# Kernel optimization log

Hardware: AMD Instinct MI355X
Metric: run time of the kernel (lower is better)

The kernel has to match this reference:

```python
import jax, jax.numpy as jnp
import numpy as np

NUM_HEADS = 8


def setup_inputs() -> dict:
    key = jax.random.key(0)
    k1, k2, k3 = jax.random.split(key, 3)
    B, N, C = 4, 2048, 256
    x = jax.random.normal(k1, (B, N, C), dtype=jnp.float32)
    qkv_w = jax.random.normal(k2, (3 * C, C), dtype=jnp.float32) * (C ** -0.5)
    proj_w = jax.random.normal(k3, (C, C), dtype=jnp.float32) * (C ** -0.5)
    proj_b = jnp.zeros((C,), dtype=jnp.float32)
    return {"x": x, "qkv_w": qkv_w, "proj_w": proj_w, "proj_b": proj_b}


def reference(x, qkv_w, proj_w, proj_b):
    B, N, C = x.shape
    H = NUM_HEADS
    hd = C // H
    scale = hd ** -0.5
    # 1x1 conv over [B,C,N,1] == per-token linear: [B,3C,N]
    qkv = jnp.einsum('bnc,dc->bdn', x, qkv_w)
    # faithful to torch reshape+chunk: per-head interleaved q/k/v layout
    qkv = qkv.reshape(B, H, 3 * hd, N)
    q, k, v = jnp.split(qkv, 3, axis=2)  # each [B,H,hd,N]
    # attn[b,h,i,j] = sum_d k[b,h,d,i] * q[b,h,d,j], scaled
    attn = jnp.einsum('bhdi,bhdj->bhij', k, q) * scale  # [B,H,Nk,Nq]
    attn = jax.nn.softmax(attn, axis=-2)  # softmax over key axis (dim=-2)
    out = jnp.einsum('bhdi,bhij->bhdj', v, attn)  # [B,H,hd,N]
    out = out.reshape(B, C, N, 1)
    # proj 1x1 conv with bias
    out = jnp.einsum('bcnq,dc->bdnq', out, proj_w) + proj_b[None, :, None, None]
    return out
```

## Files before the change

kernel.cpp:

```cpp
#include <hip/hip_runtime.h>
#include <hip/hip_bf16.h>

#define NTOK 2048
#define CDIM 256
#define HEADS 8
#define HD 32
#define QSC 0.25505480068568306f

typedef __attribute__((ext_vector_type(8))) short short8;
typedef __attribute__((ext_vector_type(4))) float float4v;
typedef unsigned short ushort_t;
typedef unsigned int uint_t;

#define MFMA(a, b, c) __builtin_amdgcn_mfma_f32_16x16x32_bf16(a, b, c, 0, 0, 0)

__device__ __forceinline__ uint_t cvt_pk(float lo, float hi) {
    uint_t r;
    asm("v_cvt_pk_bf16_f32 %0, %1, %2" : "=v"(r) : "v"(lo), "v"(hi));
    return r;
}
__device__ __forceinline__ ushort_t f2bf(float f) {
    union { __hip_bfloat16 h; ushort_t u; } cv;
    cv.h = __float2bfloat16(f);
    return cv.u;
}
#if __has_builtin(__builtin_amdgcn_exp2f)
#define EXP2(x) __builtin_amdgcn_exp2f(x)
#else
#define EXP2(x) exp2f(x)
#endif

__global__ __launch_bounds__(256) void cvt_all(const float* __restrict__ x,
                                               const float* __restrict__ w,
                                               const float* __restrict__ w2,
                                               uint4* __restrict__ xo,
                                               uint4* __restrict__ wo,
                                               uint4* __restrict__ w2o) {
    const int bid = blockIdx.x;
    const float* in; uint4* out; int i;
    if (bid < 1024)      { in = x;  out = xo;  i = bid * 256 + threadIdx.x; }
    else if (bid < 1120) { in = w;  out = wo;  i = (bid - 1024) * 256 + threadIdx.x; }
    else                 { in = w2; out = w2o; i = (bid - 1120) * 256 + threadIdx.x; }
    const float4* p = (const float4*)in + (size_t)2 * i;
    float4 a = p[0], bq = p[1];
    uint4 r;
    r.x = cvt_pk(a.x, a.y);   r.y = cvt_pk(a.z, a.w);
    r.z = cvt_pk(bq.x, bq.y); r.w = cvt_pk(bq.z, bq.w);
    out[i] = r;
}

__global__ __launch_bounds__(256) void qkv_mfma(const ushort_t* __restrict__ x_bf,
                                                const ushort_t* __restrict__ w_bf,
                                                ushort_t* __restrict__ q_t,
                                                ushort_t* __restrict__ k_t,
                                                ushort_t* __restrict__ v_) {
    __shared__ ushort_t lds[4][2048];
    const int tid = threadIdx.x, wave = tid >> 6, lane = tid & 63;
    const int l15 = lane & 15, g = lane >> 4;
    const int b = blockIdx.z;
    const int dtile = blockIdx.x * 64 + (wave >> 1) * 32;
    const int ntile = blockIdx.y * 128 + (wave & 1) * 64;

    const ushort_t* A = w_bf + (size_t)dtile * CDIM + g * 8;
    const ushort_t* B = x_bf + ((size_t)b * NTOK + ntile) * CDIM + g * 8;

    float4v acc[2][4];
    #pragma unroll
    for (int i = 0; i < 2; ++i)
        #pragma unroll
        for (int j = 0; j < 4; ++j)
            #pragma unroll
            for (int r = 0; r < 4; ++r) acc[i][j][r] = 0.f;

    #pragma unroll
    for (int k0 = 0; k0 < CDIM; k0 += 32) {
        short8 af[2], bf[4];
        #pragma unroll
        for (int i = 0; i < 2; ++i)
            af[i] = *(const short8*)&A[(size_t)(l15 + 16 * i) * CDIM + k0];
        #pragma unroll
        for (int j = 0; j < 4; ++j)
            bf[j] = *(const short8*)&B[(size_t)(l15 + 16 * j) * CDIM + k0];
        #pragma unroll
        for (int i = 0; i < 2; ++i)
            #pragma unroll
            for (int j = 0; j < 4; ++j)
                acc[i][j] = MFMA(af[i], bf[j], acc[i][j]);
    }

    const int hq = (dtile * 683) >> 16;
    const int tl = dtile - hq * 96;
    const size_t bh = (size_t)(b * HEADS + hq);
    ushort_t* W = lds[wave];

    if (tl == 64) {
        #pragma unroll
        for (int i = 0; i < 2; ++i)
            #pragma unroll
            for (int j = 0; j < 4; ++j) {
                const int c = j * 2 + (l15 >> 3);
                #pragma unroll
                for (int r = 0; r < 4; ++r) {
                    const int d = i * 16 + g * 4 + r;
                    W[d * 64 + ((c ^ (d & 7)) * 8) + (l15 & 7)] = f2bf(acc[i][j][r]);
                }
            }
        ushort_t* vb = v_ + bh * ((size_t)NTOK * HD);
        #pragma unroll
        for (int t = 0; t < 4; ++t) {
            const int d = t * 8 + (lane >> 3), c = lane & 7;
            uint4 val = *(const uint4*)&W[d * 64 + ((c ^ (d & 7)) * 8)];
            *(uint4*)&vb[(size_t)d * NTOK + ntile + c * 8] = val;
        }
    } else {
        ushort_t* base = (tl ? k_t : q_t) + bh * ((size_t)NTOK * HD);
        const float mul = tl ? 1.f : QSC;
        #pragma unroll
        for (int i = 0; i < 2; ++i)
            #pragma unroll
            for (int j = 0; j < 4; ++j) {
                uint2 pk;
                pk.x = cvt_pk(acc[i][j][0] * mul, acc[i][j][1] * mul);
                pk.y = cvt_pk(acc[i][j][2] * mul, acc[i][j][3] * mul);
                const int row = j * 16 + l15;
                const int c16 = i * 2 + (g >> 1);
                *(uint2*)&W[row * 32 + ((c16 ^ (row & 3)) * 8) + (g & 1) * 4] = pk;
            }
        #pragma unroll
        for (int t = 0; t < 4; ++t) {
            const int row = t * 16 + (lane >> 2), c = lane & 3;
            uint4 val = *(const uint4*)&W[row * 32 + ((c ^ (row & 3)) * 8)];
            *(uint4*)&base[(size_t)(ntile + row) * HD + c * 8] = val;
        }
    }
}

__global__ __launch_bounds__(256) void attn_mfma(const ushort_t* __restrict__ q_t,
                                                 const ushort_t* __restrict__ k_t,
                                                 const ushort_t* __restrict__ v_,
                                                 ushort_t* __restrict__ preT) {
    __shared__ float smem[4][1152];
    const int tid = threadIdx.x, wave = tid >> 6, lane = tid & 63;
    const int l15 = lane & 15, g = lane >> 4;
    const int bh = blockIdx.x, b = bh >> 3, h = bh & 7;
    const int j0 = blockIdx.y * 64 + (wave >> 1) * 32;
    const int khalf = wave & 1;

    const ushort_t* qb = q_t + (size_t)bh * (NTOK * HD);
    const ushort_t* kb = k_t + (size_t)bh * (NTOK * HD);
    const ushort_t* vb = v_  + (size_t)bh * (NTOK * HD);

    short8 qf0 = *(const short8*)&qb[(size_t)(j0 + l15) * HD + g * 8];
    short8 qf1 = *(const short8*)&qb[(size_t)(j0 + 16 + l15) * HD + g * 8];

    short8 ones;
    #pragma unroll
    for (int r = 0; r < 8; ++r) ones[r] = (short)0x3F80;

    const float4v z4 = {0.f, 0.f, 0.f, 0.f};
    float4v o00 = z4, o01 = z4, o10 = z4, o11 = z4;
    float4v lacc0 = z4, lacc1 = z4;

    float* myb = smem[wave];
    uint_t* pt0 = (uint_t*)myb;
    uint_t* pt1 = (uint_t*)myb + 320;
    const int wbase = l15 * 20 + g * 2;
    const int rbase = l15 * 20 + g * 4;

    const int kbeg = khalf * 1024, kend = kbeg + 1024;
    short8 aK0 = *(const short8*)&kb[(size_t)(kbeg + l15) * HD + g * 8];
    short8 aK1 = *(const short8*)&kb[(size_t)(kbeg + 16 + l15) * HD + g * 8];
    short8 aV0 = *(const short8*)&vb[(size_t)l15 * NTOK + kbeg + g * 8];
    short8 aV1 = *(const short8*)&vb[(size_t)(16 + l15) * NTOK + kbeg + g * 8];

    for (int i0 = kbeg; i0 < kend; i0 += 32) {
        const int ip = (i0 + 32 < kend) ? i0 + 32 : kbeg;
        short8 nK0 = *(const short8*)&kb[(size_t)(ip + l15) * HD + g * 8];
        short8 nK1 = *(const short8*)&kb[(size_t)(ip + 16 + l15) * HD + g * 8];
        short8 nV0 = *(const short8*)&vb[(size_t)l15 * NTOK + ip + g * 8];
        short8 nV1 = *(const short8*)&vb[(size_t)(16 + l15) * NTOK + ip + g * 8];

        float4v s00 = MFMA(aK0, qf0, z4);
        float4v s10 = MFMA(aK1, qf0, z4);
        float4v s01 = MFMA(aK0, qf1, z4);
        float4v s11 = MFMA(aK1, qf1, z4);

        uint2 w0, w1;
        w0.x = cvt_pk(EXP2(s00[0]), EXP2(s00[1]));
        w0.y = cvt_pk(EXP2(s00[2]), EXP2(s00[3]));
        w1.x = cvt_pk(EXP2(s10[0]), EXP2(s10[1]));
        w1.y = cvt_pk(EXP2(s10[2]), EXP2(s10[3]));
        *(uint2*)&pt0[wbase]     = w0;
        *(uint2*)&pt0[wbase + 8] = w1;
        w0.x = cvt_pk(EXP2(s01[0]), EXP2(s01[1]));
        w0.y = cvt_pk(EXP2(s01[2]), EXP2(s01[3]));
        w1.x = cvt_pk(EXP2(s11[0]), EXP2(s11[1]));
        w1.y = cvt_pk(EXP2(s11[2]), EXP2(s11[3]));
        *(uint2*)&pt1[wbase]     = w0;
        *(uint2*)&pt1[wbase + 8] = w1;

        short8 pB0 = *(const short8*)&pt0[rbase];
        short8 pB1 = *(const short8*)&pt1[rbase];

        lacc0 = MFMA(ones, pB0, lacc0);
        lacc1 = MFMA(ones, pB1, lacc1);
        o00 = MFMA(aV0, pB0, o00);
        o01 = MFMA(aV0, pB1, o01);
        o10 = MFMA(aV1, pB0, o10);
        o11 = MFMA(aV1, pB1, o11);

        aK0 = nK0; aK1 = nK1; aV0 = nV0; aV1 = nV1;
    }

    float* dst = &myb[lane * 18];
    #pragma unroll
    for (int r = 0; r < 4; ++r) {
        dst[r] = o00[r]; dst[4 + r] = o01[r]; dst[8 + r] = o10[r]; dst[12 + r] = o11[r];
    }
    dst[16] = lacc0[0]; dst[17] = lacc1[0];
    __syncthreads();

    if (khalf == 0) {
        const float* cp = &smem[wave ^ 1][lane * 18];
        #pragma unroll
        for (int r = 0; r < 4; ++r) {
            o00[r] += cp[r]; o01[r] += cp[4 + r]; o10[r] += cp[8 + r]; o11[r] += cp[12 + r];
        }
        const float rl0 = 1.f / (lacc0[0] + cp[16]);
        const float rl1 = 1.f / (lacc1[0] + cp[17]);

        ushort_t* pb_ = preT + ((size_t)b * NTOK + j0) * CDIM + h * HD;
        uint2 w0, w1, w2, w3;
        w0.x = cvt_pk(o00[0] * rl0, o00[1] * rl0); w0.y = cvt_pk(o00[2] * rl0, o00[3] * rl0);
        w1.x = cvt_pk(o01[0] * rl1, o01[1] * rl1); w1.y = cvt_pk(o01[2] * rl1, o01[3] * rl1);
        w2.x = cvt_pk(o10[0] * rl0, o10[1] * rl0); w2.y = cvt_pk(o10[2] * rl0, o10[3] * rl0);
        w3.x = cvt_pk(o11[0] * rl1, o11[1] * rl1); w3.y = cvt_pk(o11[2] * rl1, o11[3] * rl1);
        *(uint2*)&pb_[(size_t)l15 * CDIM + g * 4] = w0;
        *(uint2*)&pb_[(size_t)(16 + l15) * CDIM + g * 4] = w1;
        *(uint2*)&pb_[(size_t)l15 * CDIM + 16 + g * 4] = w2;
        *(uint2*)&pb_[(size_t)(16 + l15) * CDIM + 16 + g * 4] = w3;
    }
}

__global__ __launch_bounds__(256) void proj_mfma(const ushort_t* __restrict__ preT,
                                                 const ushort_t* __restrict__ w2_bf,
                                                 const float* __restrict__ pb,
                                                 float* __restrict__ out) {
    const int tid = threadIdx.x, wave = tid >> 6, lane = tid & 63;
    const int l15 = lane & 15, g = lane >> 4;
    const int b = blockIdx.z;
    const int dtile = blockIdx.x * 64 + (wave >> 1) * 32;
    const int ntile = blockIdx.y * 64 + (wave & 1) * 32;

    const ushort_t* A = w2_bf + (size_t)dtile * CDIM + g * 8;
    const ushort_t* B = preT + ((size_t)b * NTOK + ntile) * CDIM + g * 8;

    float4v acc[2][2];
    #pragma unroll
    for (int i = 0; i < 2; ++i)
        #pragma unroll
        for (int j = 0; j < 2; ++j)
            #pragma unroll
            for (int r = 0; r < 4; ++r) acc[i][j][r] = 0.f;

    #pragma unroll
    for (int k0 = 0; k0 < CDIM; k0 += 32) {
        short8 af[2], bf[2];
        #pragma unroll
        for (int i = 0; i < 2; ++i)
            af[i] = *(const short8*)&A[(size_t)(l15 + 16 * i) * CDIM + k0];
        #pragma unroll
        for (int j = 0; j < 2; ++j)
            bf[j] = *(const short8*)&B[(size_t)(l15 + 16 * j) * CDIM + k0];
        #pragma unroll
        for (int i = 0; i < 2; ++i)
            #pragma unroll
            for (int j = 0; j < 2; ++j)
                acc[i][j] = MFMA(af[i], bf[j], acc[i][j]);
    }

    #pragma unroll
    for (int i = 0; i < 2; ++i) {
        #pragma unroll
        for (int r = 0; r < 4; ++r) {
            const int d = dtile + i * 16 + g * 4 + r;
            const float bias = pb[d];
            float* orow = out + ((size_t)b * CDIM + d) * NTOK + ntile;
            #pragma unroll
            for (int j = 0; j < 2; ++j)
                orow[j * 16 + l15] = acc[i][j][r] + bias;
        }
    }
}

extern "C" void kernel_launch(void* const* d_in, const int* in_sizes, int n_in,
                              void* d_out, int out_size, void* d_ws, size_t ws_size,
                              hipStream_t stream) {
    const float* x      = (const float*)d_in[0];
    const float* qkv_w  = (const float*)d_in[1];
    const float* proj_w = (const float*)d_in[2];
    const float* proj_b = (const float*)d_in[3];
    float* out = (float*)d_out;

    char* ws = (char*)d_ws;
    ushort_t* x_bf  = (ushort_t*)(ws);
    ushort_t* preT  = (ushort_t*)(ws);
    ushort_t* w_bf  = (ushort_t*)(ws + (size_t)4 * 1024 * 1024);
    ushort_t* w2_bf = (ushort_t*)(ws + (size_t)4608 * 1024);
    ushort_t* q_t   = (ushort_t*)(ws + (size_t)5 * 1024 * 1024);
    ushort_t* k_t   = (ushort_t*)(ws + (size_t)9 * 1024 * 1024);
    ushort_t* v_    = (ushort_t*)(ws + (size_t)13 * 1024 * 1024);

    cvt_all<<<1152, 256, 0, stream>>>(x, qkv_w, proj_w,
                                      (uint4*)x_bf, (uint4*)w_bf, (uint4*)w2_bf);
    qkv_mfma<<<dim3(12, 16, 4), 256, 0, stream>>>(x_bf, w_bf, q_t, k_t, v_);
    attn_mfma<<<dim3(4 * HEADS, NTOK / 64), 256, 0, stream>>>(q_t, k_t, v_, preT);
    proj_mfma<<<dim3(4, 32, 4), 256, 0, stream>>>(preT, w2_bf, proj_b, out);
}
```

Measured before the change: 144.8 us.

## Permute V token layout so softmax probabilities feed MFMA directly from registers

The QKV projection now stores V with its token index permuted so that the MFMA output layout of the exp'd scores matches the B-operand layout needed for the PV MFMA. This removes the per-iteration LDS write/read round trip used to transpose the probability tile. The cost is more complex index math in the V-writing epilogue, and correctness depends on the permutation exactly matching the register layout, since the sum over tokens is order-invariant only if K and V stay consistent.

Measured after the change: 144.3 us. Within noise of the previous version (-0.3%).

```diff
diff --git a/kernel.cpp b/kernel.cpp
--- a/kernel.cpp
+++ b/kernel.cpp
@@ -11,6 +11,7 @@
 typedef __attribute__((ext_vector_type(4))) float float4v;
 typedef unsigned short ushort_t;
 typedef unsigned int uint_t;
+typedef __attribute__((ext_vector_type(4))) uint_t uint4v;
 
 #define MFMA(a, b, c) __builtin_amdgcn_mfma_f32_16x16x32_bf16(a, b, c, 0, 0, 0)
 
@@ -29,6 +30,15 @@
 #else
 #define EXP2(x) exp2f(x)
 #endif
+
+__device__ __forceinline__ short8 pack_p(float4v sA, float4v sB) {
+    uint4v u;
+    u[0] = cvt_pk(EXP2(sA[0]), EXP2(sA[1]));
+    u[1] = cvt_pk(EXP2(sA[2]), EXP2(sA[3]));
+    u[2] = cvt_pk(EXP2(sB[0]), EXP2(sB[1]));
+    u[3] = cvt_pk(EXP2(sB[2]), EXP2(sB[3]));
+    return __builtin_bit_cast(short8, u);
+}
 
 __global__ __launch_bounds__(256) void cvt_all(const float* __restrict__ x,
                                                const float* __restrict__ w,
@@ -98,11 +108,14 @@
         for (int i = 0; i < 2; ++i)
             #pragma unroll
             for (int j = 0; j < 4; ++j) {
-                const int c = j * 2 + (l15 >> 3);
+                const int m = (j & 1) * 16 + l15;
+                const int p = ((m & 12) << 1) + (m & 3) + ((m & 16) >> 2);
+                const int phys = (j >> 1) * 32 + p;
+                const int c = phys >> 3;
                 #pragma unroll
                 for (int r = 0; r < 4; ++r) {
                     const int d = i * 16 + g * 4 + r;
-                    W[d * 64 + ((c ^ (d & 7)) * 8) + (l15 & 7)] = f2bf(acc[i][j][r]);
+                    W[d * 64 + ((c ^ (d & 7)) * 8) + (phys & 7)] = f2bf(acc[i][j][r]);
                 }
             }
         ushort_t* vb = v_ + bh * ((size_t)NTOK * HD);
@@ -161,12 +174,6 @@
     float4v o00 = z4, o01 = z4, o10 = z4, o11 = z4;
     float4v lacc0 = z4, lacc1 = z4;
 
-    float* myb = smem[wave];
-    uint_t* pt0 = (uint_t*)myb;
-    uint_t* pt1 = (uint_t*)myb + 320;
-    const int wbase = l15 * 20 + g * 2;
-    const int rbase = l15 * 20 + g * 4;
-
     const int kbeg = khalf * 1024, kend = kbeg + 1024;
     short8 aK0 = *(const short8*)&kb[(size_t)(kbeg + l15) * HD + g * 8];
     short8 aK1 = *(const short8*)&kb[(size_t)(kbeg + 16 + l15) * HD + g * 8];
@@ -185,34 +192,20 @@
         float4v s01 = MFMA(aK0, qf1, z4);
         float4v s11 = MFMA(aK1, qf1, z4);
 
-        uint2 w0, w1;
-        w0.x = cvt_pk(EXP2(s00[0]), EXP2(s00[1]));
-        w0.y = cvt_pk(EXP2(s00[2]), EXP2(s00[3]));
-        w1.x = cvt_pk(EXP2(s10[0]), EXP2(s10[1]));
-        w1.y = cvt_pk(EXP2(s10[2]), EXP2(s10[3]));
-        *(uint2*)&pt0[wbase]     = w0;
-        *(uint2*)&pt0[wbase + 8] = w1;
-        w0.x = cvt_pk(EXP2(s01[0]), EXP2(s01[1]));
-        w0.y = cvt_pk(EXP2(s01[2]), EXP2(s01[3]));
-        w1.x = cvt_pk(EXP2(s11[0]), EXP2(s11[1]));
-        w1.y = cvt_pk(EXP2(s11[2]), EXP2(s11[3]));
-        *(uint2*)&pt1[wbase]     = w0;
-        *(uint2*)&pt1[wbase + 8] = w1;
-
-        short8 pB0 = *(const short8*)&pt0[rbase];
-        short8 pB1 = *(const short8*)&pt1[rbase];
-
-        lacc0 = MFMA(ones, pB0, lacc0);
-        lacc1 = MFMA(ones, pB1, lacc1);
-        o00 = MFMA(aV0, pB0, o00);
-        o01 = MFMA(aV0, pB1, o01);
-        o10 = MFMA(aV1, pB0, o10);
-        o11 = MFMA(aV1, pB1, o11);
+        short8 p0 = pack_p(s00, s10);
+        short8 p1 = pack_p(s01, s11);
+
+        lacc0 = MFMA(ones, p0, lacc0);
+        lacc1 = MFMA(ones, p1, lacc1);
+        o00 = MFMA(aV0, p0, o00);
+        o01 = MFMA(aV0, p1, o01);
+        o10 = MFMA(aV1, p0, o10);
+        o11 = MFMA(aV1, p1, o11);
 
         aK0 = nK0; aK1 = nK1; aV0 = nV0; aV1 = nV1;
     }
 
-    float* dst = &myb[lane * 18];
+    float* dst = &smem[wave][lane * 18];
     #pragma unroll
     for (int r = 0; r < 4; ++r) {
         dst[r] = o00[r]; dst[4 + r] = o01[r]; dst[8 + r] = o10[r]; dst[12 + r] = o11[r];
```
